# Kernel tuning notes

Measured on AMD Instinct MI355X. Metric: run time of the kernel, lower is better.

Reference implementation:

```python
import jax, jax.numpy as jnp
import numpy as np

HIDDEN = 128
STATE = 64
ACTION = 16
D_IO = STATE + ACTION  # 80
BATCH = 4096
SEQ_LEN = 512


def setup_inputs() -> dict:
    key = jax.random.key(0)
    ks = jax.random.split(key, 7)
    s = 1.0 / np.sqrt(HIDDEN)
    return {
        "quantized_hn": jax.random.normal(ks[0], (BATCH, HIDDEN), jnp.float32),
        "W_ih": jax.random.uniform(ks[1], (4 * HIDDEN, D_IO), jnp.float32, -s, s),
        "W_hh": jax.random.uniform(ks[2], (4 * HIDDEN, HIDDEN), jnp.float32, -s, s),
        "b_ih": jax.random.uniform(ks[3], (4 * HIDDEN,), jnp.float32, -s, s),
        "b_hh": jax.random.uniform(ks[4], (4 * HIDDEN,), jnp.float32, -s, s),
        "W_fc": jax.random.uniform(ks[5], (D_IO, HIDDEN), jnp.float32, -s, s),
        "b_fc": jax.random.uniform(ks[6], (D_IO,), jnp.float32, -s, s),
        "seq_len": SEQ_LEN,
    }


def reference(quantized_hn, W_ih, W_hh, b_ih, b_hh, W_fc, b_fc, seq_len):
    B, H = quantized_hn.shape
    D = W_fc.shape[0]

    def step(carry, _):
        h, c, x = carry  # h,c: (B,H); x: (B,D)
        # PyTorch LSTM gate order: i, f, g, o
        gates = x @ W_ih.T + b_ih + h @ W_hh.T + b_hh  # (B, 4H)
        i, f, g, o = jnp.split(gates, 4, axis=-1)
        c_new = jax.nn.sigmoid(f) * c + jax.nn.sigmoid(i) * jnp.tanh(g)
        h_new = jax.nn.sigmoid(o) * jnp.tanh(c_new)
        y = h_new @ W_fc.T + b_fc  # (B, D) -> fed back as next input
        return (h_new, c_new, y), y

    h0 = quantized_hn
    c0 = jnp.zeros((B, H), quantized_hn.dtype)
    x0 = jnp.zeros((B, D), quantized_hn.dtype)
    _, ys = jax.lax.scan(step, (h0, c0, x0), None, length=seq_len)
    return jnp.transpose(ys, (1, 0, 2))  # (B, seq_len, D)
```

## Files before the change

kernel.cpp:

```cpp
#include <hip/hip_runtime.h>

typedef __bf16 bf16_t;
typedef __bf16 bf16x4 __attribute__((ext_vector_type(4)));
typedef __bf16 bf16x8 __attribute__((ext_vector_type(8)));
typedef float  f32x4  __attribute__((ext_vector_type(4)));

#define HID    128
#define DIO    80
#define G4     512
#define TSTEP  512
#define BB     16
#define NBATCH 4096
#define NBLK   (NBATCH / BB)
#define HSTR   136

__device__ bf16_t g_weff_frags[128 * 512];
__device__ bf16_t g_whh_frags[128 * 512];
__device__ bf16_t g_wfc_frags[20 * 512];
__device__ float  g_weff[G4 * HID];
__device__ float  g_beff[G4];
__device__ float  g_b1[G4];

__global__ void k_weff(const float* __restrict__ W_ih, const float* __restrict__ W_hh,
                       const float* __restrict__ b_ih, const float* __restrict__ b_hh,
                       const float* __restrict__ W_fc, const float* __restrict__ b_fc) {
  int gid = blockIdx.x * blockDim.x + threadIdx.x;
  int g = gid >> 7, k = gid & 127;
  float acc = W_hh[g * HID + k];
#pragma unroll 8
  for (int d = 0; d < DIO; ++d)
    acc = fmaf(W_ih[g * DIO + d], W_fc[d * HID + k], acc);
  g_weff[g * HID + k] = acc;
  if (k == 0) {
    float bb = b_ih[g] + b_hh[g];
    g_b1[g] = bb;
    float be = bb;
    for (int d = 0; d < DIO; ++d) be = fmaf(W_ih[g * DIO + d], b_fc[d], be);
    g_beff[g] = be;
  }
}

__global__ void k_frag(const float* __restrict__ W_hh, const float* __restrict__ W_fc) {
  int tile = blockIdx.x;
  int lane = threadIdx.x;
  int c = lane & 15, q = lane >> 4;
  if (tile < 128) {
    int gtile = tile >> 2, kt = tile & 3;
    int n = gtile * 16 + c;
#pragma unroll
    for (int j = 0; j < 8; ++j)
      g_weff_frags[tile * 512 + lane * 8 + j] = (bf16_t)g_weff[n * HID + kt * 32 + q * 8 + j];
  } else if (tile < 256) {
    int t2 = tile - 128;
    int gtile = t2 >> 2, kt = t2 & 3;
    int n = gtile * 16 + c;
#pragma unroll
    for (int j = 0; j < 8; ++j)
      g_whh_frags[t2 * 512 + lane * 8 + j] = (bf16_t)W_hh[n * HID + kt * 32 + q * 8 + j];
  } else {
    int t2 = tile - 256;
    int yt = t2 >> 2, kt = t2 & 3;
    int n = yt * 16 + c;
#pragma unroll
    for (int j = 0; j < 8; ++j)
      g_wfc_frags[t2 * 512 + lane * 8 + j] = (bf16_t)W_fc[n * HID + kt * 32 + q * 8 + j];
  }
}

__device__ __forceinline__ float fsigm(float x) {
  return __builtin_amdgcn_rcpf(1.0f + __builtin_amdgcn_exp2f(x * -1.4426950408889634f));
}
__device__ __forceinline__ float ftanh(float x) {
  return 1.0f - 2.0f * __builtin_amdgcn_rcpf(1.0f + __builtin_amdgcn_exp2f(x * 2.8853900817779268f));
}

__global__ __launch_bounds__(512, 2) void k_lstm(const float* __restrict__ h0,
                                                 const float* __restrict__ b_fc,
                                                 float* __restrict__ out) {
  __shared__ __align__(16) bf16_t hbuf[2][BB * HSTR];
  const int tid = threadIdx.x;
  const int lane = tid & 63;
  const int w = tid >> 6;
  const int c = lane & 15, q = lane >> 4;
  const int b0 = blockIdx.x * BB;

  for (int i = tid; i < BB * HID; i += 512) {
    int r = i >> 7, k = i & 127;
    hbuf[0][r * HSTR + k] = (bf16_t)h0[(long)(b0 + r) * HID + k];
  }

  bf16x8 Wy[4];
  f32x4  ybias;
  if (w < 5) {
#pragma unroll
    for (int kt = 0; kt < 4; ++kt)
      Wy[kt] = *(const bf16x8*)&g_wfc_frags[(w * 4 + kt) * 512 + lane * 8];
#pragma unroll
    for (int r = 0; r < 4; ++r) ybias[r] = b_fc[w * 16 + q * 4 + r];
  }

  bf16x8 Wg[4][4];
  f32x4  bias[4];
  auto load_wg = [&](const bf16_t* frags, const float* bsrc) {
#pragma unroll
    for (int G = 0; G < 4; ++G) {
      int gtile = G * 8 + w;
#pragma unroll
      for (int r = 0; r < 4; ++r) bias[G][r] = bsrc[gtile * 16 + q * 4 + r];
#pragma unroll
      for (int kt = 0; kt < 4; ++kt)
        Wg[G][kt] = *(const bf16x8*)&frags[(gtile * 4 + kt) * 512 + lane * 8];
    }
  };

  f32x4 cst = (f32x4){0, 0, 0, 0};
  bf16x8 hf[4];

  __syncthreads();
#pragma unroll
  for (int kt = 0; kt < 4; ++kt)
    hf[kt] = *(const bf16x8*)&hbuf[0][c * HSTR + kt * 32 + q * 8];

  float* outp = out + (long)(b0 + c) * TSTEP * DIO + w * 16 + q * 4;

  auto step = [&](int t) {
    f32x4 acc[4];
#pragma unroll
    for (int G = 0; G < 4; ++G) acc[G] = bias[G];
#pragma unroll
    for (int kt = 0; kt < 4; ++kt)
#pragma unroll
      for (int G = 0; G < 4; ++G)
        acc[G] = __builtin_amdgcn_mfma_f32_16x16x32_bf16(Wg[G][kt], hf[kt], acc[G], 0, 0, 0);

    const int buf = t & 1;
    bf16x4 hv;
#pragma unroll
    for (int r = 0; r < 4; ++r) {
      float iv = fsigm(acc[0][r]);
      float fv = fsigm(acc[1][r]);
      float gv = ftanh(acc[2][r]);
      float ov = fsigm(acc[3][r]);
      float cn = fv * cst[r] + iv * gv;
      cst[r] = cn;
      hv[r] = (bf16_t)(ov * ftanh(cn));
    }
    *(bf16x4*)&hbuf[buf][c * HSTR + w * 16 + q * 4] = hv;
    __syncthreads();
#pragma unroll
    for (int kt = 0; kt < 4; ++kt)
      hf[kt] = *(const bf16x8*)&hbuf[buf][c * HSTR + kt * 32 + q * 8];

    if (w < 5) {
      f32x4 ya = ybias;
#pragma unroll
      for (int kt = 0; kt < 4; ++kt)
        ya = __builtin_amdgcn_mfma_f32_16x16x32_bf16(Wy[kt], hf[kt], ya, 0, 0, 0);
      *(f32x4*)&outp[(long)(t - 1) * DIO] = ya;
    }
  };

  load_wg(g_whh_frags, g_b1);
  step(1);
  load_wg(g_weff_frags, g_beff);
  for (int t = 2; t <= TSTEP; ++t) step(t);
}

extern "C" void kernel_launch(void* const* d_in, const int* in_sizes, int n_in,
                              void* d_out, int out_size, void* d_ws, size_t ws_size,
                              hipStream_t stream) {
  const float* h0   = (const float*)d_in[0];
  const float* W_ih = (const float*)d_in[1];
  const float* W_hh = (const float*)d_in[2];
  const float* b_ih = (const float*)d_in[3];
  const float* b_hh = (const float*)d_in[4];
  const float* W_fc = (const float*)d_in[5];
  const float* b_fc = (const float*)d_in[6];
  float* out = (float*)d_out;

  k_weff<<<256, 256, 0, stream>>>(W_ih, W_hh, b_ih, b_hh, W_fc, b_fc);
  k_frag<<<276, 64, 0, stream>>>(W_hh, W_fc);
  k_lstm<<<NBLK, 512, 0, stream>>>(h0, b_fc, out);
}
```

Measured before the change: 996.3 us.

## Fold activation scale constants into weights and share reciprocals across LSTM gates

Pre-scales the gate weights and biases by -log2(e), or by 2*log2(e) for the g gate, so each gate needs only one exp2 with no extra multiply. The cell state is kept in the scaled domain, and the sigmoid/tanh reciprocals are merged into two rcp calls per element instead of six. Alternate waves also get raised scheduling priority, the first MFMA now takes the bias directly as its accumulator, and the output pointer is advanced incrementally. The aim is a shorter transcendental chain on the serial per-step critical path, at the cost of slightly different rounding and a clamp to guard exp2 overflow.

```diff
diff --git a/kernel.cpp b/kernel.cpp
--- a/kernel.cpp
+++ b/kernel.cpp
@@ -14,6 +14,9 @@
 #define NBLK   (NBATCH / BB)
 #define HSTR   136
 
+#define NL2E  -1.4426950408889634f
+#define P2L2E  2.8853900817779268f
+
 __device__ bf16_t g_weff_frags[128 * 512];
 __device__ bf16_t g_whh_frags[128 * 512];
 __device__ bf16_t g_wfc_frags[20 * 512];
@@ -26,17 +29,18 @@
                        const float* __restrict__ W_fc, const float* __restrict__ b_fc) {
   int gid = blockIdx.x * blockDim.x + threadIdx.x;
   int g = gid >> 7, k = gid & 127;
+  float sc = ((g >> 7) == 2) ? P2L2E : NL2E;
   float acc = W_hh[g * HID + k];
 #pragma unroll 8
   for (int d = 0; d < DIO; ++d)
     acc = fmaf(W_ih[g * DIO + d], W_fc[d * HID + k], acc);
-  g_weff[g * HID + k] = acc;
+  g_weff[g * HID + k] = acc * sc;
   if (k == 0) {
     float bb = b_ih[g] + b_hh[g];
-    g_b1[g] = bb;
+    g_b1[g] = bb * sc;
     float be = bb;
     for (int d = 0; d < DIO; ++d) be = fmaf(W_ih[g * DIO + d], b_fc[d], be);
-    g_beff[g] = be;
+    g_beff[g] = be * sc;
   }
 }
 
@@ -54,9 +58,10 @@
     int t2 = tile - 128;
     int gtile = t2 >> 2, kt = t2 & 3;
     int n = gtile * 16 + c;
+    float sc = ((n >> 7) == 2) ? P2L2E : NL2E;
 #pragma unroll
     for (int j = 0; j < 8; ++j)
-      g_whh_frags[t2 * 512 + lane * 8 + j] = (bf16_t)W_hh[n * HID + kt * 32 + q * 8 + j];
+      g_whh_frags[t2 * 512 + lane * 8 + j] = (bf16_t)(W_hh[n * HID + kt * 32 + q * 8 + j] * sc);
   } else {
     int t2 = tile - 256;
     int yt = t2 >> 2, kt = t2 & 3;
@@ -65,13 +70,6 @@
     for (int j = 0; j < 8; ++j)
       g_wfc_frags[t2 * 512 + lane * 8 + j] = (bf16_t)W_fc[n * HID + kt * 32 + q * 8 + j];
   }
-}
-
-__device__ __forceinline__ float fsigm(float x) {
-  return __builtin_amdgcn_rcpf(1.0f + __builtin_amdgcn_exp2f(x * -1.4426950408889634f));
-}
-__device__ __forceinline__ float ftanh(float x) {
-  return 1.0f - 2.0f * __builtin_amdgcn_rcpf(1.0f + __builtin_amdgcn_exp2f(x * 2.8853900817779268f));
 }
 
 __global__ __launch_bounds__(512, 2) void k_lstm(const float* __restrict__ h0,
@@ -123,12 +121,15 @@
 
   float* outp = out + (long)(b0 + c) * TSTEP * DIO + w * 16 + q * 4;
 
+  if (((tid >> 6) & 1) == 0) __builtin_amdgcn_s_setprio(1);
+
   auto step = [&](int t) {
     f32x4 acc[4];
 #pragma unroll
-    for (int G = 0; G < 4; ++G) acc[G] = bias[G];
+    for (int G = 0; G < 4; ++G)
+      acc[G] = __builtin_amdgcn_mfma_f32_16x16x32_bf16(Wg[G][0], hf[0], bias[G], 0, 0, 0);
 #pragma unroll
-    for (int kt = 0; kt < 4; ++kt)
+    for (int kt = 1; kt < 4; ++kt)
 #pragma unroll
       for (int G = 0; G < 4; ++G)
         acc[G] = __builtin_amdgcn_mfma_f32_16x16x32_bf16(Wg[G][kt], hf[kt], acc[G], 0, 0, 0);
@@ -137,13 +138,22 @@
     bf16x4 hv;
 #pragma unroll
     for (int r = 0; r < 4; ++r) {
-      float iv = fsigm(acc[0][r]);
-      float fv = fsigm(acc[1][r]);
-      float gv = ftanh(acc[2][r]);
-      float ov = fsigm(acc[3][r]);
-      float cn = fv * cst[r] + iv * gv;
+      float Ei = __builtin_amdgcn_exp2f(acc[0][r]);
+      float Ef = __builtin_amdgcn_exp2f(acc[1][r]);
+      float Eg = __builtin_amdgcn_exp2f(acc[2][r]);
+      float Eo = __builtin_amdgcn_exp2f(acc[3][r]);
+      float ai = 1.0f + Ei, af = 1.0f + Ef, ag = 1.0f + Eg;
+      float P1 = ai * ag;
+      float R  = __builtin_amdgcn_rcpf(P1 * af);
+      float fs = P1 * R;
+      float tg = __builtin_fmaf(Eg, P2L2E, -P2L2E);
+      float term = tg * af * R;
+      float cn = __builtin_fmaf(fs, cst[r], term);
       cst[r] = cn;
-      hv[r] = (bf16_t)(ov * ftanh(cn));
+      float cc = fminf(cn, 80.0f);
+      float Ec = __builtin_amdgcn_exp2f(cc);
+      float R2 = __builtin_amdgcn_rcpf((1.0f + Eo) * (1.0f + Ec));
+      hv[r] = (bf16_t)((Ec - 1.0f) * R2);
     }
     *(bf16x4*)&hbuf[buf][c * HSTR + w * 16 + q * 4] = hv;
     __syncthreads();
@@ -152,11 +162,12 @@
       hf[kt] = *(const bf16x8*)&hbuf[buf][c * HSTR + kt * 32 + q * 8];
 
     if (w < 5) {
-      f32x4 ya = ybias;
+      f32x4 ya = __builtin_amdgcn_mfma_f32_16x16x32_bf16(Wy[0], hf[0], ybias, 0, 0, 0);
 #pragma unroll
-      for (int kt = 0; kt < 4; ++kt)
+      for (int kt = 1; kt < 4; ++kt)
         ya = __builtin_amdgcn_mfma_f32_16x16x32_bf16(Wy[kt], hf[kt], ya, 0, 0, 0);
-      *(f32x4*)&outp[(long)(t - 1) * DIO] = ya;
+      *(f32x4*)outp = ya;
+      outp += DIO;
     }
   };
 
```

Measured after the change: 962.0 us. -3.4%, faster.
